# Performance work log

Hardware: AMD Instinct MI355X
Metric: run time of the kernel (lower is better)

## Reference

```python
import jax, jax.numpy as jnp
import numpy as np

N_FEATS = 128
N_NODES = 100000
N_EDGES = 1000000
NUM_SEGMENTS = 4096


def setup_inputs() -> dict:
    key = jax.random.key(0)
    ks = jax.random.split(key, 10)
    glorot = lambda k, shape: jax.random.uniform(
        k, shape, dtype=jnp.float32,
        minval=-1.0, maxval=1.0) * np.sqrt(6.0 / (shape[0] + shape[1]))
    x_j = jax.random.normal(ks[0], (N_NODES, N_FEATS), dtype=jnp.float32)
    x_i = jax.random.normal(ks[1], (N_NODES, N_FEATS), dtype=jnp.float32)
    edge_index = jax.random.randint(ks[2], (2, N_EDGES), 0, N_NODES)
    edge_index_batch = jnp.sort(jax.random.randint(ks[3], (N_EDGES,), 0, NUM_SEGMENTS))
    w_j = glorot(ks[4], (N_FEATS, N_FEATS))
    w_i = glorot(ks[5], (N_FEATS, N_FEATS))
    bias = jnp.zeros((N_FEATS,), dtype=jnp.float32)
    prelu_w = jnp.array(0.25, dtype=jnp.float32)  # nn.PReLU default init
    # nn.Linear(out_feats, 1) default init: U(-1/sqrt(fan_in), 1/sqrt(fan_in))
    lim = 1.0 / np.sqrt(N_FEATS)
    mlp_W = jax.random.uniform(ks[6], (N_FEATS, 1), dtype=jnp.float32, minval=-lim, maxval=lim)
    mlp_b = jax.random.uniform(ks[7], (1,), dtype=jnp.float32, minval=-lim, maxval=lim)
    return {"x_j": x_j, "x_i": x_i, "edge_index": edge_index,
            "edge_index_batch": edge_index_batch, "w_j": w_j, "w_i": w_i,
            "bias": bias, "prelu_w": prelu_w, "mlp_W": mlp_W, "mlp_b": mlp_b}


def reference(x_j, x_i, edge_index, edge_index_batch, w_j, w_i, bias, prelu_w, mlp_W, mlp_b):
    # project node features: [N, F]
    xi = x_i @ w_i
    xj = x_j @ w_j
    # gather endpoints per edge and fuse bias add: [E, F]
    h = xj[edge_index[0]] + xi[edge_index[1]] + bias
    # PReLU (single shared slope) then Linear(F, 1) -> [E]
    h = jnp.where(h >= 0, h, prelu_w * h)
    alpha = (h @ mlp_W).reshape(-1) + mlp_b[0]
    # per-graph segmented softmax (PyG torch_geometric.utils.softmax)
    seg_max = jax.ops.segment_max(alpha, edge_index_batch, num_segments=NUM_SEGMENTS)
    e = jnp.exp(alpha - seg_max[edge_index_batch])
    seg_sum = jax.ops.segment_sum(e, edge_index_batch, num_segments=NUM_SEGMENTS)
    return e / (seg_sum[edge_index_batch] + 1e-16)
```

## Files before the change

### kernel.cpp

```cpp
#include <hip/hip_runtime.h>
#include <hip/hip_fp16.h>
#include <float.h>

#define NSEG 4096
#define CAP 2048

typedef __attribute__((ext_vector_type(8))) _Float16 half8;
typedef __attribute__((ext_vector_type(2))) _Float16 h2v;
typedef __attribute__((ext_vector_type(4))) float f32x4;

__global__ __launch_bounds__(256) void setup(
    const int* __restrict__ batch, int* __restrict__ segs, int E,
    const float* __restrict__ Wj, const float* __restrict__ Wi,
    __half* __restrict__ Wpk) {
  const int bid = blockIdx.x;
  if (bid < 17) {
    int b = bid * 256 + threadIdx.x;
    if (b > NSEG) return;
    int lo = 0, hi = E;
    while (lo < hi) { int mid = (lo + hi) >> 1; if (batch[mid] < b) lo = mid + 1; else hi = mid; }
    segs[b] = lo;
  } else {
    int tid = (bid - 17) * 256 + threadIdx.x;
    for (int idx = tid; idx < 2 * 4 * 8 * 64 * 8; idx += 32 * 256) {
      int r     = idx & 7;
      int l     = (idx >> 3) & 63;
      int nt    = (idx >> 9) & 7;
      int kt    = (idx >> 12) & 3;
      int which = idx >> 14;
      const float* W = which ? Wi : Wj;
      int k = kt * 32 + (l >> 4) * 8 + r;
      int n = nt * 16 + (l & 15);
      float v = W[k * 128 + n];
      __half hi = __float2half(v);
      __half lo = __float2half(v - __half2float(hi));
      size_t base = ((size_t)which * 32 + (size_t)(kt * 8 + nt)) * 1024;
      Wpk[base + l * 8 + r]       = hi;
      Wpk[base + 512 + l * 8 + r] = lo;
    }
  }
}

__global__ __launch_bounds__(256) void proj_mfma(
    const float* __restrict__ Xj, const float* __restrict__ Xi,
    const float* __restrict__ bias, const __half* __restrict__ Wpk,
    __half* __restrict__ Yj, __half* __restrict__ Yi, int nrows) {
  const int which = blockIdx.y;
  const float* X = which ? Xi : Xj;
  __half* Y = which ? Yi : Yj;
  const _Float16* WpkB = (const _Float16*)Wpk + (size_t)which * 32768;

  __shared__ _Float16 Wlds[2][8192];

  const int tid  = threadIdx.x;
  const int wid  = tid >> 6;
  const int lane = tid & 63;
  const int lr   = lane & 15;
  const int lg   = lane >> 4;

  const long row0 = (long)blockIdx.x * 64 + wid * 16;
  long r0 = row0 + lr;
  const float* p0 = X + (r0 < nrows ? r0 : 0) * 128 + lg * 8;

  {
    const float4* s_ = (const float4*)(WpkB);
    float4* d_ = (float4*)Wlds[0];
    d_[tid]       = s_[tid];
    d_[256 + tid] = s_[256 + tid];
    d_[512 + tid] = s_[512 + tid];
    d_[768 + tid] = s_[768 + tid];
  }
  float4 xa = *(const float4*)(p0);
  float4 xb = *(const float4*)(p0 + 4);
  float4 na = *(const float4*)(p0 + 32);
  float4 nb = *(const float4*)(p0 + 36);

  __syncthreads();

  f32x4 acc[8] = {};

#define CVT1(dsth, dstl, idx, val)                                   \
  { float v_ = (val); _Float16 h_ = (_Float16)v_;                    \
    dsth[idx] = h_; dstl[idx] = (_Float16)(v_ - (float)h_); }
#define CVT8(dsth, dstl, v0, v1)                                     \
  CVT1(dsth, dstl, 0, (v0).x) CVT1(dsth, dstl, 1, (v0).y)            \
  CVT1(dsth, dstl, 2, (v0).z) CVT1(dsth, dstl, 3, (v0).w)            \
  CVT1(dsth, dstl, 4, (v1).x) CVT1(dsth, dstl, 5, (v1).y)            \
  CVT1(dsth, dstl, 6, (v1).z) CVT1(dsth, dstl, 7, (v1).w)

#define MFMA(a, b, c) __builtin_amdgcn_mfma_f32_16x16x32_f16((a), (b), (c), 0, 0, 0)

#define KT_STEP(kt, HASN1, HASN2)                                        \
  {                                                                      \
    float4 sw0, sw1, sw2, sw3;                                           \
    if (HASN1) {                                                         \
      const float4* s_ = (const float4*)(WpkB + ((kt) + 1) * 8192);      \
      sw0 = s_[tid];                                                     \
      sw1 = s_[256 + tid];                                               \
      sw2 = s_[512 + tid];                                               \
      sw3 = s_[768 + tid];                                               \
    }                                                                    \
    half8 xh, xl;                                                        \
    CVT8(xh, xl, xa, xb);                                                \
    if (HASN1) { xa = na; xb = nb; }                                     \
    if (HASN2) {                                                         \
      na = *(const float4*)(p0 + ((kt) + 2) * 32);                       \
      nb = *(const float4*)(p0 + ((kt) + 2) * 32 + 4);                   \
    }                                                                    \
    _Pragma("unroll")                                                    \
    for (int nt = 0; nt < 8; ++nt) {                                     \
      const _Float16* f = &Wlds[(kt) & 1][nt * 1024 + lane * 8];         \
      half8 wh = *(const half8*)(f);                                     \
      half8 wl = *(const half8*)(f + 512);                               \
      acc[nt] = MFMA(wh, xh, acc[nt]);                                   \
      acc[nt] = MFMA(wh, xl, acc[nt]);                                   \
      acc[nt] = MFMA(wl, xh, acc[nt]);                                   \
    }                                                                    \
    if (HASN1) {                                                         \
      float4* d_ = (float4*)Wlds[((kt) + 1) & 1];                        \
      d_[tid]       = sw0;                                               \
      d_[256 + tid] = sw1;                                               \
      d_[512 + tid] = sw2;                                               \
      d_[768 + tid] = sw3;                                               \
      __syncthreads();                                                   \
    }                                                                    \
  }

  KT_STEP(0, 1, 1)
  KT_STEP(1, 1, 1)
  KT_STEP(2, 1, 0)
  KT_STEP(3, 0, 0)

#undef KT_STEP
#undef MFMA
#undef CVT8
#undef CVT1

  long row = row0 + lr;
  if (row < nrows) {
    __half* yr = Y + row * 128;
    #pragma unroll
    for (int nt = 0; nt < 8; ++nt) {
      float4 bv = make_float4(0.f, 0.f, 0.f, 0.f);
      if (which) bv = *(const float4*)(bias + nt * 16 + lg * 4);
      __half2 v01 = __floats2half2_rn(acc[nt][0] + bv.x, acc[nt][1] + bv.y);
      __half2 v23 = __floats2half2_rn(acc[nt][2] + bv.z, acc[nt][3] + bv.w);
      uint2 u;
      u.x = *(unsigned int*)&v01;
      u.y = *(unsigned int*)&v23;
      *(uint2*)(yr + nt * 16 + lg * 4) = u;
    }
  }
}

__global__ __launch_bounds__(256) void seg_softmax(
    const __half* __restrict__ xjp, const __half* __restrict__ xip,
    const int* __restrict__ ei, const int* __restrict__ segs,
    const float* __restrict__ mlpW, const float* __restrict__ prelu_w,
    const float* __restrict__ mlp_b, float* __restrict__ out, int E) {
  const int start = segs[blockIdx.x];
  const int end = segs[blockIdx.x + 1];
  const int cnt = end - start;
  if (cnt <= 0) return;

  __shared__ float aS[CAP];
  __shared__ float red[8];

  const int tid = threadIdx.x;
  const int lane = tid & 63;
  const int wid = tid >> 6;
  const int g   = tid >> 4;
  const int ql  = tid & 15;

  const float4 w0 = *(const float4*)(mlpW + ql * 8);
  const float4 w1 = *(const float4*)(mlpW + ql * 8 + 4);
  const float pw = prelu_w[0];
  const float mb = mlp_b[0];
  const bool useLds = (cnt <= CAP);

  const uint4* XJ = (const uint4*)xjp;
  const uint4* XI = (const uint4*)xip;
  const h2v pwv = { (_Float16)pw, (_Float16)pw };
  const h2v zv  = { (_Float16)0.f, (_Float16)0.f };

  for (int e0 = start + g * 4; e0 < end; e0 += 64) {
    const int eB = e0 + 1, eC = e0 + 2, eD = e0 + 3;
    const bool vB = (eB < end), vC = (eC < end), vD = (eD < end);
    int sA = ei[e0],            dA = ei[E + e0];
    int sB = vB ? ei[eB] : sA,  dB = vB ? ei[E + eB] : dA;
    int sC = vC ? ei[eC] : sA,  dC = vC ? ei[E + eC] : dA;
    int sD = vD ? ei[eD] : sA,  dD = vD ? ei[E + eD] : dA;

    uint4 aA = XJ[(size_t)sA * 16 + ql], bA = XI[(size_t)dA * 16 + ql];
    uint4 aB = XJ[(size_t)sB * 16 + ql], bB = XI[(size_t)dB * 16 + ql];
    uint4 aC = XJ[(size_t)sC * 16 + ql], bC = XI[(size_t)dC * 16 + ql];
    uint4 aD = XJ[(size_t)sD * 16 + ql], bD = XI[(size_t)dD * 16 + ql];

    float pA, pB, pC, pD;
#define EALPHA(av, bv, p)                                                   \
    {                                                                       \
      h2v h0 = *(h2v*)&(av).x + *(h2v*)&(bv).x;                             \
      h2v h1 = *(h2v*)&(av).y + *(h2v*)&(bv).y;                             \
      h2v h2 = *(h2v*)&(av).z + *(h2v*)&(bv).z;                             \
      h2v h3 = *(h2v*)&(av).w + *(h2v*)&(bv).w;                             \
      h0 = __builtin_elementwise_max(h0, zv)                                \
         + pwv * __builtin_elementwise_min(h0, zv);                         \
      h1 = __builtin_elementwise_max(h1, zv)                                \
         + pwv * __builtin_elementwise_min(h1, zv);                         \
      h2 = __builtin_elementwise_max(h2, zv)                                \
         + pwv * __builtin_elementwise_min(h2, zv);                         \
      h3 = __builtin_elementwise_max(h3, zv)                                \
         + pwv * __builtin_elementwise_min(h3, zv);                         \
      p = (float)h0.x * w0.x;                                               \
      p = fmaf((float)h0.y, w0.y, p); p = fmaf((float)h1.x, w0.z, p);       \
      p = fmaf((float)h1.y, w0.w, p); p = fmaf((float)h2.x, w1.x, p);       \
      p = fmaf((float)h2.y, w1.y, p); p = fmaf((float)h3.x, w1.z, p);       \
      p = fmaf((float)h3.y, w1.w, p);                                       \
    }
    EALPHA(aA, bA, pA);
    EALPHA(aB, bB, pB);
    EALPHA(aC, bC, pC);
    EALPHA(aD, bD, pD);
#undef EALPHA

    #pragma unroll
    for (int off = 1; off < 16; off <<= 1) {
      pA += __shfl_xor(pA, off, 64);
      pB += __shfl_xor(pB, off, 64);
      pC += __shfl_xor(pC, off, 64);
      pD += __shfl_xor(pD, off, 64);
    }
    if (ql == 0) {
      if (useLds) {
        aS[e0 - start] = pA + mb;
        if (vB) aS[eB - start] = pB + mb;
        if (vC) aS[eC - start] = pC + mb;
        if (vD) aS[eD - start] = pD + mb;
      } else {
        out[e0] = pA + mb;
        if (vB) out[eB] = pB + mb;
        if (vC) out[eC] = pC + mb;
        if (vD) out[eD] = pD + mb;
      }
    }
  }
  __syncthreads();

  float m = -FLT_MAX;
  if (useLds) { for (int i = tid; i < cnt; i += 256) m = fmaxf(m, aS[i]); }
  else        { for (int i = tid; i < cnt; i += 256) m = fmaxf(m, out[start + i]); }
  #pragma unroll
  for (int off = 1; off < 64; off <<= 1) m = fmaxf(m, __shfl_xor(m, off, 64));
  if (lane == 0) red[wid] = m;
  __syncthreads();
  m = fmaxf(fmaxf(red[0], red[1]), fmaxf(red[2], red[3]));

  float s = 0.f;
  if (useLds) {
    for (int i = tid; i < cnt; i += 256) { float x = expf(aS[i] - m); aS[i] = x; s += x; }
  } else {
    for (int i = tid; i < cnt; i += 256) { float x = expf(out[start + i] - m); out[start + i] = x; s += x; }
  }
  #pragma unroll
  for (int off = 1; off < 64; off <<= 1) s += __shfl_xor(s, off, 64);
  if (lane == 0) red[4 + wid] = s;
  __syncthreads();
  s = (red[4] + red[5]) + (red[6] + red[7]);

  const float inv = 1.0f / (s + 1e-16f);
  if (useLds) { for (int i = tid; i < cnt; i += 256) out[start + i] = aS[i] * inv; }
  else        { for (int i = tid; i < cnt; i += 256) out[start + i] *= inv; }
}

extern "C" void kernel_launch(void* const* d_in, const int* in_sizes, int n_in,
                              void* d_out, int out_size, void* d_ws, size_t ws_size,
                              hipStream_t stream) {
  const float* x_j      = (const float*)d_in[0];
  const float* x_i      = (const float*)d_in[1];
  const int*   edge_idx = (const int*)d_in[2];
  const int*   batch    = (const int*)d_in[3];
  const float* w_j      = (const float*)d_in[4];
  const float* w_i      = (const float*)d_in[5];
  const float* bias     = (const float*)d_in[6];
  const float* prelu_w  = (const float*)d_in[7];
  const float* mlp_W    = (const float*)d_in[8];
  const float* mlp_b    = (const float*)d_in[9];
  const int nnodes = in_sizes[0] / 128;
  const int E = in_sizes[3];

  __half* Wpk = (__half*)d_ws;
  __half* xjp = Wpk + 65536;
  __half* xip = xjp + (size_t)nnodes * 128;
  int* segs   = (int*)(xip + (size_t)nnodes * 128);

  hipLaunchKernelGGL(setup, dim3(49), dim3(256), 0, stream,
                     batch, segs, E, w_j, w_i, Wpk);

  int gblocks = (nnodes + 63) / 64;
  hipLaunchKernelGGL(proj_mfma, dim3(gblocks, 2), dim3(256), 0, stream,
                     x_j, x_i, bias, Wpk, xjp, xip, nnodes);

  hipLaunchKernelGGL(seg_softmax, dim3(NSEG), dim3(256), 0, stream,
                     xjp, xip, edge_idx, segs, mlp_W, prelu_w, mlp_b,
                     (float*)d_out, E);
}
```

Measured before the change: 243.0 us.

## Make projection kernel persistent with resident weights and prefetched row tiles

The projection GEMM now uses a fixed grid of 256x2 persistent blocks of 512 threads. Each block loads the full packed hi/lo fp16 weight matrix (64KB) into LDS once, then loops over 128-row tiles and prefetches the next tile's inputs into registers while computing the current one. This removes the per-block weight reloads and the in-loop double-buffer syncs of the old 64-row-per-block design. In exchange it uses more registers and LDS per block, which lowers occupancy, and there are fewer blocks to hide memory latency.

```diff
diff --git a/kernel.cpp b/kernel.cpp
--- a/kernel.cpp
+++ b/kernel.cpp
@@ -41,16 +41,15 @@
   }
 }
 
-__global__ __launch_bounds__(256) void proj_mfma(
+__global__ __launch_bounds__(512) void proj_mfma(
     const float* __restrict__ Xj, const float* __restrict__ Xi,
     const float* __restrict__ bias, const __half* __restrict__ Wpk,
     __half* __restrict__ Yj, __half* __restrict__ Yi, int nrows) {
   const int which = blockIdx.y;
   const float* X = which ? Xi : Xj;
   __half* Y = which ? Yi : Yj;
-  const _Float16* WpkB = (const _Float16*)Wpk + (size_t)which * 32768;
-
-  __shared__ _Float16 Wlds[2][8192];
+
+  __shared__ _Float16 Wlds[32768];
 
   const int tid  = threadIdx.x;
   const int wid  = tid >> 6;
@@ -58,26 +57,30 @@
   const int lr   = lane & 15;
   const int lg   = lane >> 4;
 
-  const long row0 = (long)blockIdx.x * 64 + wid * 16;
-  long r0 = row0 + lr;
-  const float* p0 = X + (r0 < nrows ? r0 : 0) * 128 + lg * 8;
-
   {
-    const float4* s_ = (const float4*)(WpkB);
-    float4* d_ = (float4*)Wlds[0];
-    d_[tid]       = s_[tid];
-    d_[256 + tid] = s_[256 + tid];
-    d_[512 + tid] = s_[512 + tid];
-    d_[768 + tid] = s_[768 + tid];
-  }
-  float4 xa = *(const float4*)(p0);
-  float4 xb = *(const float4*)(p0 + 4);
-  float4 na = *(const float4*)(p0 + 32);
-  float4 nb = *(const float4*)(p0 + 36);
-
-  __syncthreads();
-
-  f32x4 acc[8] = {};
+    const float4* src = (const float4*)(Wpk + (size_t)which * 32768);
+    float4* dst = (float4*)Wlds;
+    #pragma unroll
+    for (int it = 0; it < 8; ++it)
+      dst[it * 512 + tid] = src[it * 512 + tid];
+  }
+
+  const int ntiles = (nrows + 127) >> 7;
+  const int NB = gridDim.x;
+
+  int tile = blockIdx.x;
+  float4 cur[8], nxt[8];
+  if (tile < ntiles) {
+    long r = (long)tile * 128 + wid * 16 + lr;
+    const float* p = X + (r < nrows ? r : 0) * 128 + lg * 8;
+    #pragma unroll
+    for (int kt = 0; kt < 4; ++kt) {
+      cur[2 * kt]     = *(const float4*)(p + kt * 32);
+      cur[2 * kt + 1] = *(const float4*)(p + kt * 32 + 4);
+    }
+  }
+
+  __syncthreads();
 
 #define CVT1(dsth, dstl, idx, val)                                   \
   { float v_ = (val); _Float16 h_ = (_Float16)v_;                    \
@@ -90,67 +93,58 @@
 
 #define MFMA(a, b, c) __builtin_amdgcn_mfma_f32_16x16x32_f16((a), (b), (c), 0, 0, 0)
 
-#define KT_STEP(kt, HASN1, HASN2)                                        \
-  {                                                                      \
-    float4 sw0, sw1, sw2, sw3;                                           \
-    if (HASN1) {                                                         \
-      const float4* s_ = (const float4*)(WpkB + ((kt) + 1) * 8192);      \
-      sw0 = s_[tid];                                                     \
-      sw1 = s_[256 + tid];                                               \
-      sw2 = s_[512 + tid];                                               \
-      sw3 = s_[768 + tid];                                               \
-    }                                                                    \
-    half8 xh, xl;                                                        \
-    CVT8(xh, xl, xa, xb);                                                \
-    if (HASN1) { xa = na; xb = nb; }                                     \
-    if (HASN2) {                                                         \
-      na = *(const float4*)(p0 + ((kt) + 2) * 32);                       \
-      nb = *(const float4*)(p0 + ((kt) + 2) * 32 + 4);                   \
-    }                                                                    \
-    _Pragma("unroll")                                                    \
-    for (int nt = 0; nt < 8; ++nt) {                                     \
-      const _Float16* f = &Wlds[(kt) & 1][nt * 1024 + lane * 8];         \
-      half8 wh = *(const half8*)(f);                                     \
-      half8 wl = *(const half8*)(f + 512);                               \
-      acc[nt] = MFMA(wh, xh, acc[nt]);                                   \
-      acc[nt] = MFMA(wh, xl, acc[nt]);                                   \
-      acc[nt] = MFMA(wl, xh, acc[nt]);                                   \
-    }                                                                    \
-    if (HASN1) {                                                         \
-      float4* d_ = (float4*)Wlds[((kt) + 1) & 1];                        \
-      d_[tid]       = sw0;                                               \
-      d_[256 + tid] = sw1;                                               \
-      d_[512 + tid] = sw2;                                               \
-      d_[768 + tid] = sw3;                                               \
-      __syncthreads();                                                   \
-    }                                                                    \
-  }
-
-  KT_STEP(0, 1, 1)
-  KT_STEP(1, 1, 1)
-  KT_STEP(2, 1, 0)
-  KT_STEP(3, 0, 0)
-
-#undef KT_STEP
+  while (tile < ntiles) {
+    const int tnext = tile + NB;
+    if (tnext < ntiles) {
+      long r = (long)tnext * 128 + wid * 16 + lr;
+      const float* p = X + (r < nrows ? r : 0) * 128 + lg * 8;
+      #pragma unroll
+      for (int kt = 0; kt < 4; ++kt) {
+        nxt[2 * kt]     = *(const float4*)(p + kt * 32);
+        nxt[2 * kt + 1] = *(const float4*)(p + kt * 32 + 4);
+      }
+    }
+
+    f32x4 acc[8] = {};
+    #pragma unroll
+    for (int kt = 0; kt < 4; ++kt) {
+      half8 xh, xl;
+      CVT8(xh, xl, cur[2 * kt], cur[2 * kt + 1]);
+      #pragma unroll
+      for (int nt = 0; nt < 8; ++nt) {
+        const _Float16* f = &Wlds[(kt * 8 + nt) * 1024 + lane * 8];
+        half8 wh = *(const half8*)(f);
+        half8 wl = *(const half8*)(f + 512);
+        acc[nt] = MFMA(wh, xh, acc[nt]);
+        acc[nt] = MFMA(wh, xl, acc[nt]);
+        acc[nt] = MFMA(wl, xh, acc[nt]);
+      }
+    }
+
+    long row = (long)tile * 128 + wid * 16 + lr;
+    if (row < nrows) {
+      __half* yr = Y + row * 128;
+      #pragma unroll
+      for (int nt = 0; nt < 8; ++nt) {
+        float4 bv = make_float4(0.f, 0.f, 0.f, 0.f);
+        if (which) bv = *(const float4*)(bias + nt * 16 + lg * 4);
+        __half2 v01 = __floats2half2_rn(acc[nt][0] + bv.x, acc[nt][1] + bv.y);
+        __half2 v23 = __floats2half2_rn(acc[nt][2] + bv.z, acc[nt][3] + bv.w);
+        uint2 u;
+        u.x = *(unsigned int*)&v01;
+        u.y = *(unsigned int*)&v23;
+        *(uint2*)(yr + nt * 16 + lg * 4) = u;
+      }
+    }
+
+    #pragma unroll
+    for (int i = 0; i < 8; ++i) cur[i] = nxt[i];
+    tile = tnext;
+  }
+
 #undef MFMA
 #undef CVT8
 #undef CVT1
-
-  long row = row0 + lr;
-  if (row < nrows) {
-    __half* yr = Y + row * 128;
-    #pragma unroll
-    for (int nt = 0; nt < 8; ++nt) {
-      float4 bv = make_float4(0.f, 0.f, 0.f, 0.f);
-      if (which) bv = *(const float4*)(bias + nt * 16 + lg * 4);
-      __half2 v01 = __floats2half2_rn(acc[nt][0] + bv.x, acc[nt][1] + bv.y);
-      __half2 v23 = __floats2half2_rn(acc[nt][2] + bv.z, acc[nt][3] + bv.w);
-      uint2 u;
-      u.x = *(unsigned int*)&v01;
-      u.y = *(unsigned int*)&v23;
-      *(uint2*)(yr + nt * 16 + lg * 4) = u;
-    }
-  }
 }
 
 __global__ __launch_bounds__(256) void seg_softmax(
@@ -296,8 +290,7 @@
   hipLaunchKernelGGL(setup, dim3(49), dim3(256), 0, stream,
                      batch, segs, E, w_j, w_i, Wpk);
 
-  int gblocks = (nnodes + 63) / 64;
-  hipLaunchKernelGGL(proj_mfma, dim3(gblocks, 2), dim3(256), 0, stream,
+  hipLaunchKernelGGL(proj_mfma, dim3(256, 2), dim3(512), 0, stream,
                      x_j, x_i, bias, Wpk, xjp, xip, nnodes);
 
   hipLaunchKernelGGL(seg_softmax, dim3(NSEG), dim3(256), 0, stream,
```

Result: slower. 321.6 us (+32.4%).
